# Performance work log

Hardware: AMD Instinct MI355X
Metric: run time of the kernel (lower is better)

## Reference

```python
import jax, jax.numpy as jnp
import numpy as np

# Instant-NGP / tcnn hash grid encoding constants (from init_kwargs)
L = 16           # n_levels
F = 2            # n_features_per_level
T = 2 ** 15      # hashmap size per level
DIM = 3
BASE = 16.0      # base_resolution
FINEST = 512.0   # finest_resolution
RANGE = 1.0
B = (FINEST / BASE) ** (1.0 / (L - 1))  # per_level_scale
N_POINTS = 500000
# tcnn spatial hash primes (first dim uses 1)
PRIMES = jnp.array([1, 2654435761, 805459861], dtype=jnp.uint32)


def setup_inputs() -> dict:
    key = jax.random.key(0)
    k1, k2 = jax.random.split(key)
    x = jax.random.uniform(k1, (N_POINTS, DIM), dtype=jnp.float32)  # points in [0,1)
    table = jax.random.normal(k2, (L, T, F), dtype=jnp.float32) * 1e-4  # tcnn-style tiny init
    return {"x": x, "table": table}


def reference(x, table):
    # wrapper: map from [-range, range] to [0, 1]
    xn = (x + RANGE) / (2.0 * RANGE)                       # [N, 3]
    n = xn.shape[0]
    # per-level grid scale (tcnn: scale = base * b^l - 1)
    scales = BASE * (B ** jnp.arange(L, dtype=jnp.float32)) - 1.0  # [L]
    pos = xn[:, None, :] * scales[None, :, None] + 0.5     # [N, L, 3]
    pos_floor = jnp.floor(pos)
    frac = pos - pos_floor                                  # [N, L, 3]
    grid = pos_floor.astype(jnp.uint32)                    # [N, L, 3]
    # 8 cube corners as binary offsets
    corners = jnp.array([[(c >> d) & 1 for d in range(DIM)] for c in range(2 ** DIM)],
                        dtype=jnp.uint32)                   # [8, 3]
    coords = grid[:, :, None, :] + corners[None, None, :, :]  # [N, L, 8, 3] uint32
    h = coords * PRIMES                                     # uint32 wraps (modular mult)
    idx = (h[..., 0] ^ h[..., 1] ^ h[..., 2]) & jnp.uint32(T - 1)  # [N, L, 8]
    # gather per-level features: [N, L, 8, F]
    feats = table[jnp.arange(L)[None, :, None], idx]
    # trilinear interpolation weights
    cf = corners.astype(jnp.float32)                        # [8, 3]
    w = jnp.prod(jnp.where(cf[None, None, :, :] == 1.0,
                           frac[:, :, None, :],
                           1.0 - frac[:, :, None, :]), axis=-1)  # [N, L, 8]
    out = jnp.einsum('nlc,nlcf->nlf', w, feats)             # [N, L, F]
    return out.reshape(n, L * F)
```

## Files before the change

kernel.cpp:

```cpp
#include <hip/hip_runtime.h>
#include <hip/hip_fp16.h>
#include <stdint.h>


constexpr int      kL  = 16;
constexpr int      kT  = 32768;
constexpr uint32_t kM  = kT - 1;
constexpr uint32_t kP1 = 2654435761u;
constexpr uint32_t kP2 = 805459861u;
constexpr int      kNC = 16;
constexpr int      kBT = 1024;

typedef float f32x2 __attribute__((ext_vector_type(2)));
typedef __attribute__((address_space(3))) uint32_t u32_lds;

__device__ __constant__ float c_scales[kL] = {
    15.0f,
    19.158736798317972f,
    24.398416831491190f,
    31.0f,
    39.317473596635944f,
    49.796833662982380f,
    63.0f,
    79.634947193271890f,
    100.59366732596477f,
    127.0f,
    160.26989438654378f,
    202.18733465192953f,
    255.0f,
    321.53978877308750f,
    405.37466930385903f,
    511.0f
};

__device__ __forceinline__ void load3c(float (&v)[3], const float* __restrict__ x,
                                       int n, int nmax) {
    int m = min(n, nmax);
    v[0] = x[m * 3 + 0];
    v[1] = x[m * 3 + 1];
    v[2] = x[m * 3 + 2];
}

__device__ __forceinline__ void hash_addr(
    uint32_t lbase, float A, float C, const float (&xv)[3],
    float (&fr)[3], uint32_t (&adr)[8])
{
    float p0 = fmaf(xv[0], A, C);
    float p1 = fmaf(xv[1], A, C);
    float p2 = fmaf(xv[2], A, C);

    float fl0 = floorf(p0), fl1 = floorf(p1), fl2 = floorf(p2);
    fr[0] = p0 - fl0;  fr[1] = p1 - fl1;  fr[2] = p2 - fl2;

    uint32_t g0 = (uint32_t)(int)fl0;
    uint32_t g1 = (uint32_t)(int)fl1;
    uint32_t g2 = (uint32_t)(int)fl2;

    uint32_t g0p = g0 + 1u;
    uint32_t hy0 = g1 * kP1;  uint32_t hy1 = hy0 + kP1;
    uint32_t hz0 = g2 * kP2;  uint32_t hz1 = hz0 + kP2;

    uint32_t hyz0 = hy0 ^ hz0;
    uint32_t hyz1 = hy1 ^ hz0;
    uint32_t hyz2 = hy0 ^ hz1;
    uint32_t hyz3 = hy1 ^ hz1;

    adr[0] = lbase + (((g0  ^ hyz0) & kM) << 2);
    adr[1] = lbase + (((g0p ^ hyz0) & kM) << 2);
    adr[2] = lbase + (((g0  ^ hyz1) & kM) << 2);
    adr[3] = lbase + (((g0p ^ hyz1) & kM) << 2);
    adr[4] = lbase + (((g0  ^ hyz2) & kM) << 2);
    adr[5] = lbase + (((g0p ^ hyz2) & kM) << 2);
    adr[6] = lbase + (((g0  ^ hyz3) & kM) << 2);
    adr[7] = lbase + (((g0p ^ hyz3) & kM) << 2);
}

__device__ __forceinline__ void issue_asm8(const uint32_t (&adr)[8], uint32_t (&e)[8]) {
    asm volatile(
        "ds_read_b32 %0, %8\n\t"
        "ds_read_b32 %1, %9\n\t"
        "ds_read_b32 %2, %10\n\t"
        "ds_read_b32 %3, %11\n\t"
        "ds_read_b32 %4, %12\n\t"
        "ds_read_b32 %5, %13\n\t"
        "ds_read_b32 %6, %14\n\t"
        "ds_read_b32 %7, %15"
        : "=&v"(e[0]), "=&v"(e[1]), "=&v"(e[2]), "=&v"(e[3]),
          "=&v"(e[4]), "=&v"(e[5]), "=&v"(e[6]), "=&v"(e[7])
        : "v"(adr[0]), "v"(adr[1]), "v"(adr[2]), "v"(adr[3]),
          "v"(adr[4]), "v"(adr[5]), "v"(adr[6]), "v"(adr[7]));
}

__device__ __forceinline__ void weights8(const float (&fr)[3], float (&wf)[8]) {
    float wx0 = 1.0f - fr[0];
    float wy0 = 1.0f - fr[1];
    float wz0 = 1.0f - fr[2];
    float wyz0 = wy0   * wz0;
    float wyz1 = fr[1] * wz0;
    float wyz2 = wy0   * fr[2];
    float wyz3 = fr[1] * fr[2];
    wf[0] = wx0   * wyz0;  wf[1] = fr[0] * wyz0;
    wf[2] = wx0   * wyz1;  wf[3] = fr[0] * wyz1;
    wf[4] = wx0   * wyz2;  wf[5] = fr[0] * wyz2;
    wf[6] = wx0   * wyz3;  wf[7] = fr[0] * wyz3;
}

__device__ __forceinline__ f32x2 consume8(const uint32_t (&e)[8], const float (&wf)[8]) {
    __half2 acc = __float2half2_rn(0.0f);
#pragma unroll
    for (int cc = 0; cc < 8; ++cc) {
        __half2 h = *reinterpret_cast<const __half2*>(&e[cc]);
        acc = __hfma2(__float2half2_rn(wf[cc]), h, acc);
    }
    f32x2 r;
    r.x = __low2float(acc);
    r.y = __high2float(acc);
    return r;
}

template<bool GUARD>
__device__ __forceinline__ void pipe_body(
    uint32_t lbase, float A, float C,
    const float* __restrict__ x, f32x2* __restrict__ out,
    int n, int l, int lim, int nmax,
    float (&frCur)[3], uint32_t (&eCur)[8],
    const float (&xIss)[3], float (&frNew)[3], uint32_t (&eNew)[8],
    float (&xPref)[3])
{
    uint32_t adr[8];
    hash_addr(lbase, A, C, xIss, frNew, adr);
    issue_asm8(adr, eNew);
    __builtin_amdgcn_sched_barrier(0);

    float wf[8];
    weights8(frCur, wf);
    load3c(xPref, x, n + 2 * kBT, nmax);

    asm volatile("s_waitcnt lgkmcnt(8)" ::: "memory");
    __builtin_amdgcn_sched_barrier(0);
    f32x2 r = consume8(eCur, wf);
    if (!GUARD || n < lim) out[(size_t)n * kL + l] = r;
}

__device__ __forceinline__ void epilogue(
    const float (&fr)[3], const uint32_t (&e)[8],
    f32x2* __restrict__ out, int n, int l, int lim)
{
    float wf[8];
    weights8(fr, wf);
    asm volatile("s_waitcnt lgkmcnt(0)" ::: "memory");
    __builtin_amdgcn_sched_barrier(0);
    f32x2 r = consume8(e, wf);
    if (n < lim) out[(size_t)n * kL + l] = r;
}

__global__ __launch_bounds__(kBT, 4) void hashgrid_fwd(
    const float*  __restrict__ x,
    const float2* __restrict__ table,
    f32x2*        __restrict__ out,
    int n_points, int chunk_sz)
{
    __shared__ uint32_t ltab[kT];

    int bid = blockIdx.x;
    int l   = bid >> 4;
    int c   = bid & 15;

    const float4* tsrc4 = reinterpret_cast<const float4*>(table + (size_t)l * kT);
    for (int e = threadIdx.x; e < kT / 2; e += kBT) {
        float4 q = tsrc4[e];
        uint2 pp;
        pp.x = ((uint32_t)__half_as_ushort(__float2half_rn(q.y)) << 16)
             |  (uint32_t)__half_as_ushort(__float2half_rn(q.x));
        pp.y = ((uint32_t)__half_as_ushort(__float2half_rn(q.w)) << 16)
             |  (uint32_t)__half_as_ushort(__float2half_rn(q.z));
        *reinterpret_cast<uint2*>(&ltab[e * 2]) = pp;
    }
    __syncthreads();

    uint32_t lbase = (uint32_t)(uintptr_t)(u32_lds*)ltab;

    float s = c_scales[l];
    float A = s * 0.5f;
    float C = fmaf(s, 0.5f, 0.5f);

    int tid  = (int)threadIdx.x;
    int base = c * chunk_sz;
    int lim  = min(base + chunk_sz, n_points);
    int nmax = n_points - 1;

    int span  = lim - base;
    int rows  = (span + kBT - 1) / kBT;
    int main2 = (rows - 1) & ~1;

    float    xA[3], xB[3], frA[3], frB[3];
    uint32_t eA[8], eB[8];

    int n = base + tid;
    load3c(xA, x, n,       nmax);
    load3c(xB, x, n + kBT, nmax);
    {
        uint32_t adr[8];
        hash_addr(lbase, A, C, xA, frA, adr);
        issue_asm8(adr, eA);
    }

    for (int r = 0; r < main2; r += 2) {
        pipe_body<false>(lbase, A, C, x, out, n,       l, lim, nmax,
                         frA, eA, xB, frB, eB, xA);
        pipe_body<false>(lbase, A, C, x, out, n + kBT, l, lim, nmax,
                         frB, eB, xA, frA, eA, xB);
        n += 2 * kBT;
    }

    if (main2 != rows - 1) {
        pipe_body<true>(lbase, A, C, x, out, n, l, lim, nmax,
                        frA, eA, xB, frB, eB, xA);
        epilogue(frB, eB, out, n + kBT, l, lim);
    } else {
        epilogue(frA, eA, out, n, l, lim);
    }
}

extern "C" void kernel_launch(void* const* d_in, const int* in_sizes, int n_in,
                              void* d_out, int out_size, void* d_ws, size_t ws_size,
                              hipStream_t stream) {
    const float*  x     = (const float*)d_in[0];
    const float2* table = (const float2*)d_in[1];
    f32x2*        out   = (f32x2*)d_out;

    int n_points = in_sizes[0] / 3;
    int chunk_sz = (n_points + kNC - 1) / kNC;
    int blocks   = kL * kNC;

    hashgrid_fwd<<<blocks, kBT, 0, stream>>>(x, table, out, n_points, chunk_sz);
}
```

Before: 50.73 us.

## Triple-buffer point loads with asm waits and overlap with table staging

Point coordinate loads move to inline-asm global loads that are issued before the LDS table staging. A rotating three-slot buffer prefetches three rows ahead, paced by explicit vmcnt waits. The main loop is unrolled six times, uses an incrementing output pointer with asm stores, and hands leftover rows to a simple serial tail loop. The aim is to hide global-load latency behind the table fill and the LDS gathers. The price is correctness that depends on hand-counted vmcnt values and a slower non-pipelined remainder path.

```diff
diff --git a/kernel.cpp b/kernel.cpp
--- a/kernel.cpp
+++ b/kernel.cpp
@@ -13,6 +13,8 @@
 
 typedef float f32x2 __attribute__((ext_vector_type(2)));
 typedef __attribute__((address_space(3))) uint32_t u32_lds;
+
+struct X3 { f32x2 xy; float z; };
 
 __device__ __constant__ float c_scales[kL] = {
     15.0f,
@@ -33,46 +35,18 @@
     511.0f
 };
 
-__device__ __forceinline__ void load3c(float (&v)[3], const float* __restrict__ x,
-                                       int n, int nmax) {
-    int m = min(n, nmax);
-    v[0] = x[m * 3 + 0];
-    v[1] = x[m * 3 + 1];
-    v[2] = x[m * 3 + 2];
-}
-
-__device__ __forceinline__ void hash_addr(
-    uint32_t lbase, float A, float C, const float (&xv)[3],
-    float (&fr)[3], uint32_t (&adr)[8])
-{
-    float p0 = fmaf(xv[0], A, C);
-    float p1 = fmaf(xv[1], A, C);
-    float p2 = fmaf(xv[2], A, C);
-
-    float fl0 = floorf(p0), fl1 = floorf(p1), fl2 = floorf(p2);
-    fr[0] = p0 - fl0;  fr[1] = p1 - fl1;  fr[2] = p2 - fl2;
-
-    uint32_t g0 = (uint32_t)(int)fl0;
-    uint32_t g1 = (uint32_t)(int)fl1;
-    uint32_t g2 = (uint32_t)(int)fl2;
-
-    uint32_t g0p = g0 + 1u;
-    uint32_t hy0 = g1 * kP1;  uint32_t hy1 = hy0 + kP1;
-    uint32_t hz0 = g2 * kP2;  uint32_t hz1 = hz0 + kP2;
-
-    uint32_t hyz0 = hy0 ^ hz0;
-    uint32_t hyz1 = hy1 ^ hz0;
-    uint32_t hyz2 = hy0 ^ hz1;
-    uint32_t hyz3 = hy1 ^ hz1;
-
-    adr[0] = lbase + (((g0  ^ hyz0) & kM) << 2);
-    adr[1] = lbase + (((g0p ^ hyz0) & kM) << 2);
-    adr[2] = lbase + (((g0  ^ hyz1) & kM) << 2);
-    adr[3] = lbase + (((g0p ^ hyz1) & kM) << 2);
-    adr[4] = lbase + (((g0  ^ hyz2) & kM) << 2);
-    adr[5] = lbase + (((g0p ^ hyz2) & kM) << 2);
-    adr[6] = lbase + (((g0  ^ hyz3) & kM) << 2);
-    adr[7] = lbase + (((g0p ^ hyz3) & kM) << 2);
+__device__ __forceinline__ void xload_asm(const float* p, X3& v) {
+    asm volatile("global_load_dwordx2 %0, %2, off\n\t"
+                 "global_load_dword %1, %2, off offset:8"
+                 : "=&v"(v.xy), "=&v"(v.z)
+                 : "v"(p)
+                 : "memory");
+}
+
+__device__ __forceinline__ void store_asm(void* p, f32x2 r) {
+    asm volatile("global_store_dwordx2 %0, %1, off"
+                 :: "v"(p), "v"(r)
+                 : "memory");
 }
 
 __device__ __forceinline__ void issue_asm8(const uint32_t (&adr)[8], uint32_t (&e)[8]) {
@@ -91,6 +65,47 @@
           "v"(adr[4]), "v"(adr[5]), "v"(adr[6]), "v"(adr[7]));
 }
 
+#define WAIT_VM4   do { asm volatile("s_waitcnt vmcnt(4)" ::: "memory"); \
+                        __builtin_amdgcn_sched_barrier(0); } while (0)
+#define WAIT_LGKM8 do { asm volatile("s_waitcnt lgkmcnt(8)" ::: "memory"); \
+                        __builtin_amdgcn_sched_barrier(0); } while (0)
+#define WAIT_LGKM0 do { asm volatile("s_waitcnt lgkmcnt(0)" ::: "memory"); \
+                        __builtin_amdgcn_sched_barrier(0); } while (0)
+
+__device__ __forceinline__ void hash_addr(
+    uint32_t lbase, float A, float Cc, const X3& xv,
+    float (&fr)[3], uint32_t (&adr)[8])
+{
+    float p0 = fmaf(xv.xy.x, A, Cc);
+    float p1 = fmaf(xv.xy.y, A, Cc);
+    float p2 = fmaf(xv.z,    A, Cc);
+
+    float fl0 = floorf(p0), fl1 = floorf(p1), fl2 = floorf(p2);
+    fr[0] = p0 - fl0;  fr[1] = p1 - fl1;  fr[2] = p2 - fl2;
+
+    uint32_t g0 = (uint32_t)(int)fl0;
+    uint32_t g1 = (uint32_t)(int)fl1;
+    uint32_t g2 = (uint32_t)(int)fl2;
+
+    uint32_t g0p = g0 + 1u;
+    uint32_t hy0 = g1 * kP1;  uint32_t hy1 = hy0 + kP1;
+    uint32_t hz0 = g2 * kP2;  uint32_t hz1 = hz0 + kP2;
+
+    uint32_t hyz0 = hy0 ^ hz0;
+    uint32_t hyz1 = hy1 ^ hz0;
+    uint32_t hyz2 = hy0 ^ hz1;
+    uint32_t hyz3 = hy1 ^ hz1;
+
+    adr[0] = lbase + (((g0  ^ hyz0) & kM) << 2);
+    adr[1] = lbase + (((g0p ^ hyz0) & kM) << 2);
+    adr[2] = lbase + (((g0  ^ hyz1) & kM) << 2);
+    adr[3] = lbase + (((g0p ^ hyz1) & kM) << 2);
+    adr[4] = lbase + (((g0  ^ hyz2) & kM) << 2);
+    adr[5] = lbase + (((g0p ^ hyz2) & kM) << 2);
+    adr[6] = lbase + (((g0  ^ hyz3) & kM) << 2);
+    adr[7] = lbase + (((g0p ^ hyz3) & kM) << 2);
+}
+
 __device__ __forceinline__ void weights8(const float (&fr)[3], float (&wf)[8]) {
     float wx0 = 1.0f - fr[0];
     float wy0 = 1.0f - fr[1];
@@ -118,40 +133,29 @@
     return r;
 }
 
-template<bool GUARD>
-__device__ __forceinline__ void pipe_body(
-    uint32_t lbase, float A, float C,
-    const float* __restrict__ x, f32x2* __restrict__ out,
-    int n, int l, int lim, int nmax,
-    float (&frCur)[3], uint32_t (&eCur)[8],
-    const float (&xIss)[3], float (&frNew)[3], uint32_t (&eNew)[8],
-    float (&xPref)[3])
+__device__ __forceinline__ void body(
+    uint32_t lbase, float A, float Cc,
+    const float* __restrict__ x, int& n, int nmax, char*& op,
+    const X3& xHash, X3& xFree,
+    float (&frC)[3], uint32_t (&eC)[8],
+    float (&frN)[3], uint32_t (&eN)[8])
 {
+    WAIT_VM4;
     uint32_t adr[8];
-    hash_addr(lbase, A, C, xIss, frNew, adr);
-    issue_asm8(adr, eNew);
+    hash_addr(lbase, A, Cc, xHash, frN, adr);
+    issue_asm8(adr, eN);
     __builtin_amdgcn_sched_barrier(0);
 
+    xload_asm(x + 3 * (size_t)min(n + 3 * kBT, nmax), xFree);
     float wf[8];
-    weights8(frCur, wf);
-    load3c(xPref, x, n + 2 * kBT, nmax);
-
-    asm volatile("s_waitcnt lgkmcnt(8)" ::: "memory");
-    __builtin_amdgcn_sched_barrier(0);
-    f32x2 r = consume8(eCur, wf);
-    if (!GUARD || n < lim) out[(size_t)n * kL + l] = r;
-}
-
-__device__ __forceinline__ void epilogue(
-    const float (&fr)[3], const uint32_t (&e)[8],
-    f32x2* __restrict__ out, int n, int l, int lim)
-{
-    float wf[8];
-    weights8(fr, wf);
-    asm volatile("s_waitcnt lgkmcnt(0)" ::: "memory");
-    __builtin_amdgcn_sched_barrier(0);
-    f32x2 r = consume8(e, wf);
-    if (n < lim) out[(size_t)n * kL + l] = r;
+    weights8(frC, wf);
+
+    WAIT_LGKM8;
+    f32x2 r = consume8(eC, wf);
+    store_asm(op, r);
+
+    n  += kBT;
+    op += (size_t)kBT * kL * sizeof(f32x2);
 }
 
 __global__ __launch_bounds__(kBT, 4) void hashgrid_fwd(
@@ -166,8 +170,19 @@
     int l   = bid >> 4;
     int c   = bid & 15;
 
+    int tid  = (int)threadIdx.x;
+    int base = c * chunk_sz;
+    int lim  = min(base + chunk_sz, n_points);
+    int nmax = n_points - 1;
+
+    int n = base + tid;
+    X3 xS0, xS1, xS2;
+    xload_asm(x + 3 * (size_t)min(n,           nmax), xS0);
+    xload_asm(x + 3 * (size_t)min(n +     kBT, nmax), xS1);
+    xload_asm(x + 3 * (size_t)min(n + 2 * kBT, nmax), xS2);
+
     const float4* tsrc4 = reinterpret_cast<const float4*>(table + (size_t)l * kT);
-    for (int e = threadIdx.x; e < kT / 2; e += kBT) {
+    for (int e = tid; e < kT / 2; e += kBT) {
         float4 q = tsrc4[e];
         uint2 pp;
         pp.x = ((uint32_t)__half_as_ushort(__float2half_rn(q.y)) << 16)
@@ -179,46 +194,58 @@
     __syncthreads();
 
     uint32_t lbase = (uint32_t)(uintptr_t)(u32_lds*)ltab;
-
-    float s = c_scales[l];
-    float A = s * 0.5f;
-    float C = fmaf(s, 0.5f, 0.5f);
-
-    int tid  = (int)threadIdx.x;
-    int base = c * chunk_sz;
-    int lim  = min(base + chunk_sz, n_points);
-    int nmax = n_points - 1;
+    float s  = c_scales[l];
+    float A  = s * 0.5f;
+    float Cc = fmaf(s, 0.5f, 0.5f);
 
     int span  = lim - base;
     int rows  = (span + kBT - 1) / kBT;
-    int main2 = (rows - 1) & ~1;
-
-    float    xA[3], xB[3], frA[3], frB[3];
+    int iters = rows - 1;
+    int sext  = iters / 6;
+
+    float    frA[3], frB[3];
     uint32_t eA[8], eB[8];
 
-    int n = base + tid;
-    load3c(xA, x, n,       nmax);
-    load3c(xB, x, n + kBT, nmax);
     {
         uint32_t adr[8];
-        hash_addr(lbase, A, C, xA, frA, adr);
+        hash_addr(lbase, A, Cc, xS0, frA, adr);
         issue_asm8(adr, eA);
     }
 
-    for (int r = 0; r < main2; r += 2) {
-        pipe_body<false>(lbase, A, C, x, out, n,       l, lim, nmax,
-                         frA, eA, xB, frB, eB, xA);
-        pipe_body<false>(lbase, A, C, x, out, n + kBT, l, lim, nmax,
-                         frB, eB, xA, frA, eA, xB);
-        n += 2 * kBT;
-    }
-
-    if (main2 != rows - 1) {
-        pipe_body<true>(lbase, A, C, x, out, n, l, lim, nmax,
-                        frA, eA, xB, frB, eB, xA);
-        epilogue(frB, eB, out, n + kBT, l, lim);
-    } else {
-        epilogue(frA, eA, out, n, l, lim);
+    char* op = (char*)(out + (size_t)n * kL + l);
+
+    for (int t = 0; t < sext; ++t) {
+        body(lbase, A, Cc, x, n, nmax, op, xS1, xS0, frA, eA, frB, eB);
+        body(lbase, A, Cc, x, n, nmax, op, xS2, xS1, frB, eB, frA, eA);
+        body(lbase, A, Cc, x, n, nmax, op, xS0, xS2, frA, eA, frB, eB);
+        body(lbase, A, Cc, x, n, nmax, op, xS1, xS0, frB, eB, frA, eA);
+        body(lbase, A, Cc, x, n, nmax, op, xS2, xS1, frA, eA, frB, eB);
+        body(lbase, A, Cc, x, n, nmax, op, xS0, xS2, frB, eB, frA, eA);
+    }
+
+    {
+        float wf[8];
+        weights8(frA, wf);
+        WAIT_LGKM0;
+        f32x2 r = consume8(eA, wf);
+        if (n < lim) out[(size_t)n * kL + l] = r;
+        n += kBT;
+    }
+
+    for (; n < lim; n += kBT) {
+        X3 xv;
+        int m = min(n, nmax);
+        xv.xy.x = x[m * 3 + 0];
+        xv.xy.y = x[m * 3 + 1];
+        xv.z    = x[m * 3 + 2];
+        float frv[3]; uint32_t adr[8], ev[8];
+        hash_addr(lbase, A, Cc, xv, frv, adr);
+        issue_asm8(adr, ev);
+        float wf[8];
+        weights8(frv, wf);
+        WAIT_LGKM0;
+        f32x2 r = consume8(ev, wf);
+        out[(size_t)n * kL + l] = r;
     }
 }
 
```

After: 50.01 us. Within noise of the previous version (-1.4%).
